# Kernel optimization log

Hardware: AMD Instinct MI355X
Metric: run time of the kernel (lower is better)

The kernel has to match this reference:

```python
import jax, jax.numpy as jnp
import numpy as np


def graph_conv(x, W, b, src, dst, n_nodes):
    """DGL GraphConv, norm='both', activation=relu.
    Pre-scale by out-degree^-1/2 of src, project (in>out so project first),
    sum-aggregate over edges, post-scale by in-degree^-1/2 of dst."""
    ones = jnp.ones(src.shape[0], dtype=x.dtype)
    deg_out = jax.ops.segment_sum(ones, src, num_segments=n_nodes)
    deg_in = jax.ops.segment_sum(ones, dst, num_segments=n_nodes)
    norm_src = jnp.clip(deg_out, 1.0, None) ** -0.5  # [N]
    norm_dst = jnp.clip(deg_in, 1.0, None) ** -0.5   # [N]
    h = x * norm_src[:, None]
    h = h @ W  # project first since in_feats > out_feats
    # message passing: gather src features, scatter-add into dst
    agg = jax.ops.segment_sum(h[src], dst, num_segments=n_nodes)  # [N, out]
    agg = agg * norm_dst[:, None]
    return jax.nn.relu(agg + b)


def setup_inputs() -> dict:
    key = jax.random.key(0)
    ks = jax.random.split(key, 6)
    N, E, D_IN, D_HID = 50000, 800000, 1024, 256
    x = jax.random.normal(ks[0], (N, D_IN), dtype=jnp.float32)
    src = jax.random.randint(ks[1], (E,), 0, N)
    dst = jax.random.randint(ks[2], (E,), 0, N)
    # Glorot-style init for weights
    W1 = jax.random.normal(ks[3], (D_IN, D_HID), dtype=jnp.float32) * (1.0 / np.sqrt(D_IN))
    b1 = jnp.zeros((D_HID,), dtype=jnp.float32)
    W2 = jax.random.normal(ks[4], (D_HID, 1), dtype=jnp.float32) * (1.0 / np.sqrt(D_HID))
    b2 = jnp.zeros((1,), dtype=jnp.float32)
    return {"x": x, "src": src, "dst": dst, "W1": W1, "b1": b1, "W2": W2, "b2": b2, "n_nodes": N}


def reference(x, src, dst, W1, b1, W2, b2, n_nodes):
    h = graph_conv(x, W1, b1, src, dst, n_nodes)   # [N, 256]
    out = graph_conv(h, W2, b2, src, dst, n_nodes)  # [N, 1]
    return out
```

## Files before the change

kernel.cpp:

```cpp
#include <hip/hip_runtime.h>
#include <hip/hip_bf16.h>

typedef __attribute__((ext_vector_type(8))) short bf16x8;
typedef __attribute__((ext_vector_type(4))) float f32x4;

static __device__ __forceinline__ short f2bf(float f) {
    unsigned u = __float_as_uint(f);
    unsigned r = (u + 0x7FFFu + ((u >> 16) & 1u)) >> 16;
    return (short)(unsigned short)r;
}
static __device__ __forceinline__ float bf2f(short s) {
    return __uint_as_float(((unsigned)(unsigned short)s) << 16);
}

static __device__ __forceinline__ void gload16(const void* g, void* l) {
    __builtin_amdgcn_global_load_lds((const __attribute__((address_space(1))) unsigned int*)g,
                                     (__attribute__((address_space(3))) unsigned int*)l, 16, 0, 0);
}

static __device__ __forceinline__ bf16x8 cvt8(const float4 lo, const float4 hi) {
    __hip_bfloat162 p0 = __float22bfloat162_rn(make_float2(lo.x, lo.y));
    __hip_bfloat162 p1 = __float22bfloat162_rn(make_float2(lo.z, lo.w));
    __hip_bfloat162 p2 = __float22bfloat162_rn(make_float2(hi.x, hi.y));
    __hip_bfloat162 p3 = __float22bfloat162_rn(make_float2(hi.z, hi.w));
    short2 s0 = *(short2*)&p0, s1 = *(short2*)&p1, s2 = *(short2*)&p2, s3 = *(short2*)&p3;
    bf16x8 r = {s0.x, s0.y, s1.x, s1.y, s2.x, s2.y, s3.x, s3.y};
    return r;
}

__global__ void deg_kernel(const int* __restrict__ src, const int* __restrict__ dst,
                           int* __restrict__ deg_out, int* __restrict__ deg_in, int E) {
    int e = blockIdx.x * blockDim.x + threadIdx.x;
    if (e < E) {
        atomicAdd(&deg_out[src[e]], 1);
        atomicAdd(&deg_in[dst[e]], 1);
    }
}

__global__ void norm_kernel(const int* __restrict__ deg_out, const int* __restrict__ deg_in,
                            float* __restrict__ ns, float* __restrict__ nd, int N) {
    int i = blockIdx.x * blockDim.x + threadIdx.x;
    if (i < N) {
        ns[i] = rsqrtf((float)max(deg_out[i], 1));
        nd[i] = rsqrtf((float)max(deg_in[i], 1));
    }
}

__global__ void scan_part1(const int* __restrict__ deg, int* __restrict__ bsum, int N) {
    __shared__ int red[256];
    int i = blockIdx.x * 256 + threadIdx.x;
    red[threadIdx.x] = (i < N) ? deg[i] : 0;
    __syncthreads();
    for (int off = 128; off > 0; off >>= 1) {
        if (threadIdx.x < off) red[threadIdx.x] += red[threadIdx.x + off];
        __syncthreads();
    }
    if (threadIdx.x == 0) bsum[blockIdx.x] = red[0];
}

__global__ void scan_part2(const int* __restrict__ bsum, int* __restrict__ bsum_ex, int NB,
                           int* __restrict__ offsets, int N, int E) {
    __shared__ int s[256];
    int t = threadIdx.x;
    int v = (t < NB) ? bsum[t] : 0;
    s[t] = v;
    __syncthreads();
    for (int off = 1; off < 256; off <<= 1) {
        int u = (t >= off) ? s[t - off] : 0;
        __syncthreads();
        s[t] += u;
        __syncthreads();
    }
    bsum_ex[t] = s[t] - v;
    if (t == 0) offsets[N] = E;
}

__global__ void scan_part3(const int* __restrict__ deg, const int* __restrict__ bsum_ex,
                           int* __restrict__ offsets, int N) {
    __shared__ int s[256];
    int t = threadIdx.x, i = blockIdx.x * 256 + t;
    int v = (i < N) ? deg[i] : 0;
    s[t] = v;
    __syncthreads();
    for (int off = 1; off < 256; off <<= 1) {
        int u = (t >= off) ? s[t - off] : 0;
        __syncthreads();
        s[t] += u;
        __syncthreads();
    }
    if (i < N) offsets[i] = bsum_ex[blockIdx.x] + s[t] - v;
}

__global__ void scatter_kernel(const int* __restrict__ src, const int* __restrict__ dst,
                               const int* __restrict__ offsets, int* __restrict__ cursor,
                               int* __restrict__ bucket, int E) {
    int e = blockIdx.x * blockDim.x + threadIdx.x;
    if (e < E) {
        int d = dst[e];
        int p = atomicAdd(&cursor[d], 1);
        bucket[offsets[d] + p] = src[e];
    }
}

__global__ __launch_bounds__(1024) void transpose_w1(const float* __restrict__ W1,
                                                     short* __restrict__ Wt) {
    __shared__ short tile[32][33];
    int k0 = blockIdx.x * 32, n0 = blockIdx.y * 32;
    int tx = threadIdx.x & 31, ty = threadIdx.x >> 5;
    tile[ty][tx] = f2bf(W1[(size_t)(k0 + ty) * 256 + (n0 + tx)]);
    __syncthreads();
    Wt[(size_t)(n0 + ty) * 1024 + (k0 + tx)] = tile[tx][ty];
}

#define BM 64
#define BN 128
#define BK 32
#define CSTR 136

union SMem {
    struct {
        short A[BM * BK];
        short B[BN * BK];
    } s;
    short C[BM * CSTR];
};

__global__ __launch_bounds__(256, 6) void gemm1_kernel(const float* __restrict__ x,
                                                       const short* __restrict__ Wt,
                                                       const float* __restrict__ norm_src,
                                                       short* __restrict__ hb, int M) {
    __shared__ __align__(16) SMem sm;
    __shared__ float ns_lds[BM];
    const int tid  = threadIdx.x;
    const int lane = tid & 63;
    const int wave = tid >> 6;
    const int quad = lane >> 4;
    const int mrow = lane & 15;
    const int wm = (wave >> 1) * 32;
    const int wn = (wave & 1) * 64;
    const int bm = blockIdx.x * BM;
    const int bn = blockIdx.y * BN;

    if (tid < BM) ns_lds[tid] = norm_src[min(bm + tid, M - 1)];

    f32x4 acc[2][4] = {};

    const int a_row = tid >> 2;
    const int a_chk = tid & 3;
    const float* a_src = x + (size_t)min(bm + a_row, M - 1) * 1024 + a_chk * 8;
    const bool a_ok = (bm + a_row < M);

    float4 a_lo, a_hi;
    a_lo = a_ok ? *(const float4*)(a_src + 0) : make_float4(0.f, 0.f, 0.f, 0.f);
    a_hi = a_ok ? *(const float4*)(a_src + 4) : make_float4(0.f, 0.f, 0.f, 0.f);

    for (int k0 = 0; k0 < 1024; k0 += BK) {
#pragma unroll
        for (int i = 0; i < 2; i++) {
            int nbase = wave * 32 + i * 16;
            int n = nbase + (lane >> 2);
            gload16(Wt + (size_t)(bn + n) * 1024 + k0 + (lane & 3) * 8, &sm.s.B[nbase * 32]);
        }
        *(bf16x8*)&sm.s.A[a_row * 32 + a_chk * 8] = cvt8(a_lo, a_hi);
        __syncthreads();

        if (k0 + BK < 1024) {
            a_lo = a_ok ? *(const float4*)(a_src + k0 + BK + 0) : make_float4(0.f, 0.f, 0.f, 0.f);
            a_hi = a_ok ? *(const float4*)(a_src + k0 + BK + 4) : make_float4(0.f, 0.f, 0.f, 0.f);
        }

        bf16x8 af[2], bfr[4];
#pragma unroll
        for (int mi = 0; mi < 2; mi++)
            af[mi] = *(const bf16x8*)&sm.s.A[(wm + mi * 16 + mrow) * 32 + quad * 8];
#pragma unroll
        for (int ni = 0; ni < 4; ni++)
            bfr[ni] = *(const bf16x8*)&sm.s.B[(wn + ni * 16 + mrow) * 32 + quad * 8];
#pragma unroll
        for (int mi = 0; mi < 2; mi++)
#pragma unroll
            for (int ni = 0; ni < 4; ni++)
                acc[mi][ni] = __builtin_amdgcn_mfma_f32_16x16x32_bf16(af[mi], bfr[ni], acc[mi][ni], 0, 0, 0);
        __syncthreads();
    }

#pragma unroll
    for (int mi = 0; mi < 2; mi++) {
#pragma unroll
        for (int reg = 0; reg < 4; reg++) {
            int row = wm + mi * 16 + quad * 4 + reg;
            float nsv = ns_lds[row];
#pragma unroll
            for (int ni = 0; ni < 4; ni++) {
                int col = wn + ni * 16 + mrow;
                sm.C[row * CSTR + col] = f2bf(acc[mi][ni][reg] * nsv);
            }
        }
    }
    __syncthreads();
#pragma unroll
    for (int j = 0; j < 4; j++) {
        int row = (tid >> 4) + j * 16;
        int chunk = tid & 15;
        if (bm + row < M) {
            int4 v = *(const int4*)&sm.C[row * CSTR + chunk * 8];
            *(int4*)(hb + (size_t)(bm + row) * 256 + bn + chunk * 8) = v;
        }
    }
}

__global__ __launch_bounds__(256) void agg1_kernel(const short* __restrict__ hb,
                                                   const int* __restrict__ bucket,
                                                   const int* __restrict__ offsets,
                                                   const float* __restrict__ norm_dst,
                                                   const float* __restrict__ norm_src,
                                                   const float* __restrict__ b1,
                                                   const float* __restrict__ W2,
                                                   float* __restrict__ z, int N) {
    int wave = threadIdx.x >> 6;
    int lane = threadIdx.x & 63;
    int node = blockIdx.x * 4 + wave;
    if (node >= N) return;
    int beg = offsets[node], end = offsets[node + 1];
    float a0 = 0.f, a1 = 0.f, a2 = 0.f, a3 = 0.f;
    int e = beg;
    for (; e + 7 < end; e += 8) {
        short4 v[8];
#pragma unroll
        for (int j = 0; j < 8; j++)
            v[j] = *(const short4*)(hb + (size_t)bucket[e + j] * 256 + lane * 4);
#pragma unroll
        for (int j = 0; j < 8; j++) {
            a0 += bf2f(v[j].x); a1 += bf2f(v[j].y);
            a2 += bf2f(v[j].z); a3 += bf2f(v[j].w);
        }
    }
    for (; e < end; e++) {
        short4 v0 = *(const short4*)(hb + (size_t)bucket[e] * 256 + lane * 4);
        a0 += bf2f(v0.x); a1 += bf2f(v0.y); a2 += bf2f(v0.z); a3 += bf2f(v0.w);
    }
    float nd = norm_dst[node];
    float4 bb = *(const float4*)(b1 + lane * 4);
    float o0 = fmaxf(a0 * nd + bb.x, 0.f);
    float o1 = fmaxf(a1 * nd + bb.y, 0.f);
    float o2 = fmaxf(a2 * nd + bb.z, 0.f);
    float o3 = fmaxf(a3 * nd + bb.w, 0.f);
    float4 w = *(const float4*)(W2 + lane * 4);
    float p = o0 * w.x + o1 * w.y + o2 * w.z + o3 * w.w;
#pragma unroll
    for (int off = 32; off > 0; off >>= 1) p += __shfl_xor(p, off, 64);
    if (lane == 0) z[node] = p * norm_src[node];
}

__global__ void agg2_kernel(const float* __restrict__ z, const int* __restrict__ bucket,
                            const int* __restrict__ offsets, const float* __restrict__ norm_dst,
                            const float* __restrict__ b2, float* __restrict__ out, int N) {
    int i = blockIdx.x * blockDim.x + threadIdx.x;
    if (i >= N) return;
    int beg = offsets[i], end = offsets[i + 1];
    float s = 0.f;
    for (int e = beg; e < end; e++) s += z[bucket[e]];
    out[i] = fmaxf(s * norm_dst[i] + b2[0], 0.f);
}

extern "C" void kernel_launch(void* const* d_in, const int* in_sizes, int n_in,
                              void* d_out, int out_size, void* d_ws, size_t ws_size,
                              hipStream_t stream) {
    const int D_HID = in_sizes[4];
    const int D_IN  = in_sizes[3] / D_HID;
    const int N     = in_sizes[0] / D_IN;
    const int E     = in_sizes[1];

    const float* x   = (const float*)d_in[0];
    const int*   src = (const int*)d_in[1];
    const int*   dst = (const int*)d_in[2];
    const float* W1  = (const float*)d_in[3];
    const float* b1  = (const float*)d_in[4];
    const float* W2  = (const float*)d_in[5];
    const float* b2  = (const float*)d_in[6];
    float* out = (float*)d_out;

    char* p = (char*)d_ws;
    auto alloc = [&](size_t bytes) {
        void* r = (void*)p;
        p += (bytes + 255) & ~(size_t)255;
        return r;
    };
    int*   deg_out  = (int*)alloc((size_t)N * 4);
    int*   deg_in   = (int*)alloc((size_t)N * 4);
    int*   cursor   = (int*)alloc((size_t)N * 4);
    float* norm_src = (float*)alloc((size_t)N * 4);
    float* norm_dst = (float*)alloc((size_t)N * 4);
    int*   offsets  = (int*)alloc((size_t)(N + 1) * 4);
    int*   bucket   = (int*)alloc((size_t)E * 4);
    short* Wt       = (short*)alloc((size_t)D_IN * D_HID * 2);
    short* hb       = (short*)alloc((size_t)N * D_HID * 2);
    float* z        = (float*)alloc((size_t)N * 4);
    int*   bsum     = (int*)alloc(256 * 4);
    int*   bsum_ex  = (int*)alloc(256 * 4);

    const int NB = (N + 255) / 256;

    hipMemsetAsync(deg_out, 0, (size_t)N * 4, stream);
    hipMemsetAsync(deg_in,  0, (size_t)N * 4, stream);
    hipMemsetAsync(cursor,  0, (size_t)N * 4, stream);

    deg_kernel<<<(E + 255) / 256, 256, 0, stream>>>(src, dst, deg_out, deg_in, E);
    norm_kernel<<<(N + 255) / 256, 256, 0, stream>>>(deg_out, deg_in, norm_src, norm_dst, N);
    scan_part1<<<NB, 256, 0, stream>>>(deg_in, bsum, N);
    scan_part2<<<1, 256, 0, stream>>>(bsum, bsum_ex, NB, offsets, N, E);
    scan_part3<<<NB, 256, 0, stream>>>(deg_in, bsum_ex, offsets, N);
    scatter_kernel<<<(E + 255) / 256, 256, 0, stream>>>(src, dst, offsets, cursor, bucket, E);
    transpose_w1<<<dim3(D_IN / 32, D_HID / 32), 1024, 0, stream>>>(W1, Wt);
    gemm1_kernel<<<dim3((N + BM - 1) / BM, D_HID / BN), 256, 0, stream>>>(x, Wt, norm_src, hb, N);
    agg1_kernel<<<(N + 3) / 4, 256, 0, stream>>>(hb, bucket, offsets, norm_dst, norm_src, b1, W2, z, N);
    agg2_kernel<<<(N + 255) / 256, 256, 0, stream>>>(z, bucket, offsets, norm_dst, b2, out, N);
}
```

Before: 526.2 us.

## Load full-width x tile once per block and stream W1 from registers

New measurement: 558.8 us. 1.06x slower.

```diff
diff --git a/kernel.cpp b/kernel.cpp
--- a/kernel.cpp
+++ b/kernel.cpp
@@ -12,12 +12,10 @@
 static __device__ __forceinline__ float bf2f(short s) {
     return __uint_as_float(((unsigned)(unsigned short)s) << 16);
 }
-
-static __device__ __forceinline__ void gload16(const void* g, void* l) {
-    __builtin_amdgcn_global_load_lds((const __attribute__((address_space(1))) unsigned int*)g,
-                                     (__attribute__((address_space(3))) unsigned int*)l, 16, 0, 0);
-}
-
+static __device__ __forceinline__ float4 nt_load4(const float* p) {
+    f32x4 v = __builtin_nontemporal_load((const f32x4*)p);
+    return make_float4(v[0], v[1], v[2], v[3]);
+}
 static __device__ __forceinline__ bf16x8 cvt8(const float4 lo, const float4 hi) {
     __hip_bfloat162 p0 = __float22bfloat162_rn(make_float2(lo.x, lo.y));
     __hip_bfloat162 p1 = __float22bfloat162_rn(make_float2(lo.z, lo.w));
@@ -112,20 +110,15 @@
     Wt[(size_t)(n0 + ty) * 1024 + (k0 + tx)] = tile[tx][ty];
 }
 
-#define BM 64
-#define BN 128
-#define BK 32
-#define CSTR 136
+#define BM 32
+#define CSTR 264
 
 union SMem {
-    struct {
-        short A[BM * BK];
-        short B[BN * BK];
-    } s;
+    short A[BM * 1024];
     short C[BM * CSTR];
 };
 
-__global__ __launch_bounds__(256, 6) void gemm1_kernel(const float* __restrict__ x,
+__global__ __launch_bounds__(256, 2) void gemm1_kernel(const float* __restrict__ x,
                                                        const short* __restrict__ Wt,
                                                        const float* __restrict__ norm_src,
                                                        short* __restrict__ hb, int M) {
@@ -136,59 +129,75 @@
     const int wave = tid >> 6;
     const int quad = lane >> 4;
     const int mrow = lane & 15;
-    const int wm = (wave >> 1) * 32;
-    const int wn = (wave & 1) * 64;
-    const int bm = blockIdx.x * BM;
-    const int bn = blockIdx.y * BN;
+    const int bm   = blockIdx.x * BM;
 
     if (tid < BM) ns_lds[tid] = norm_src[min(bm + tid, M - 1)];
 
+#pragma unroll
+    for (int half = 0; half < 2; half++) {
+        float4 lo[8], hi[8];
+#pragma unroll
+        for (int t = 0; t < 8; t++) {
+            int idx = half * 8 + t;
+            int r   = wave * 8 + (idx >> 1);
+            int s   = idx & 1;
+            const float* p = x + (size_t)min(bm + r, M - 1) * 1024 + s * 512 + lane * 8;
+            lo[t] = nt_load4(p);
+            hi[t] = nt_load4(p + 4);
+        }
+#pragma unroll
+        for (int t = 0; t < 8; t++) {
+            int idx = half * 8 + t;
+            int r   = wave * 8 + (idx >> 1);
+            int s   = idx & 1;
+            int c   = s * 64 + lane;
+            int cs  = c ^ (r & 7);
+            *(bf16x8*)((char*)sm.A + r * 2048 + cs * 16) = cvt8(lo[t], hi[t]);
+        }
+    }
+    __syncthreads();
+
     f32x4 acc[2][4] = {};
-
-    const int a_row = tid >> 2;
-    const int a_chk = tid & 3;
-    const float* a_src = x + (size_t)min(bm + a_row, M - 1) * 1024 + a_chk * 8;
-    const bool a_ok = (bm + a_row < M);
-
-    float4 a_lo, a_hi;
-    a_lo = a_ok ? *(const float4*)(a_src + 0) : make_float4(0.f, 0.f, 0.f, 0.f);
-    a_hi = a_ok ? *(const float4*)(a_src + 4) : make_float4(0.f, 0.f, 0.f, 0.f);
-
-    for (int k0 = 0; k0 < 1024; k0 += BK) {
-#pragma unroll
-        for (int i = 0; i < 2; i++) {
-            int nbase = wave * 32 + i * 16;
-            int n = nbase + (lane >> 2);
-            gload16(Wt + (size_t)(bn + n) * 1024 + k0 + (lane & 3) * 8, &sm.s.B[nbase * 32]);
-        }
-        *(bf16x8*)&sm.s.A[a_row * 32 + a_chk * 8] = cvt8(a_lo, a_hi);
-        __syncthreads();
-
-        if (k0 + BK < 1024) {
-            a_lo = a_ok ? *(const float4*)(a_src + k0 + BK + 0) : make_float4(0.f, 0.f, 0.f, 0.f);
-            a_hi = a_ok ? *(const float4*)(a_src + k0 + BK + 4) : make_float4(0.f, 0.f, 0.f, 0.f);
-        }
-
-        bf16x8 af[2], bfr[4];
+    const int wn = wave * 64;
+    const short* wB = Wt + (size_t)(wn + mrow) * 1024 + quad * 8;
+
+    bf16x8 bA[2][2], bB[2][4];
+#pragma unroll
+    for (int ni = 0; ni < 4; ni++)
+        bB[0][ni] = *(const bf16x8*)(wB + (size_t)ni * 16 * 1024);
+#pragma unroll
+    for (int mi = 0; mi < 2; mi++) {
+        int r = mi * 16 + mrow;
+        bA[0][mi] = *(const bf16x8*)((char*)sm.A + r * 2048 + ((quad ^ (r & 7)) * 16));
+    }
+
+    for (int k0 = 0; k0 < 1024; k0 += 32) {
+        int cur = (k0 >> 5) & 1, nxt = cur ^ 1;
+        if (k0 + 32 < 1024) {
+            int k1 = k0 + 32;
+#pragma unroll
+            for (int ni = 0; ni < 4; ni++)
+                bB[nxt][ni] = *(const bf16x8*)(wB + (size_t)ni * 16 * 1024 + k1);
+#pragma unroll
+            for (int mi = 0; mi < 2; mi++) {
+                int r = mi * 16 + mrow;
+                int c = (k1 >> 3) + quad;
+                bA[nxt][mi] = *(const bf16x8*)((char*)sm.A + r * 2048 + ((c ^ (r & 7)) * 16));
+            }
+        }
 #pragma unroll
         for (int mi = 0; mi < 2; mi++)
-            af[mi] = *(const bf16x8*)&sm.s.A[(wm + mi * 16 + mrow) * 32 + quad * 8];
-#pragma unroll
-        for (int ni = 0; ni < 4; ni++)
-            bfr[ni] = *(const bf16x8*)&sm.s.B[(wn + ni * 16 + mrow) * 32 + quad * 8];
-#pragma unroll
-        for (int mi = 0; mi < 2; mi++)
 #pragma unroll
             for (int ni = 0; ni < 4; ni++)
-                acc[mi][ni] = __builtin_amdgcn_mfma_f32_16x16x32_bf16(af[mi], bfr[ni], acc[mi][ni], 0, 0, 0);
-        __syncthreads();
-    }
-
+                acc[mi][ni] = __builtin_amdgcn_mfma_f32_16x16x32_bf16(bA[cur][mi], bB[cur][ni], acc[mi][ni], 0, 0, 0);
+    }
+
+    __syncthreads();
 #pragma unroll
     for (int mi = 0; mi < 2; mi++) {
 #pragma unroll
         for (int reg = 0; reg < 4; reg++) {
-            int row = wm + mi * 16 + quad * 4 + reg;
+            int row = mi * 16 + quad * 4 + reg;
             float nsv = ns_lds[row];
 #pragma unroll
             for (int ni = 0; ni < 4; ni++) {
@@ -198,13 +207,15 @@
         }
     }
     __syncthreads();
-#pragma unroll
-    for (int j = 0; j < 4; j++) {
-        int row = (tid >> 4) + j * 16;
-        int chunk = tid & 15;
+    {
+        int row = tid >> 3;
         if (bm + row < M) {
-            int4 v = *(const int4*)&sm.C[row * CSTR + chunk * 8];
-            *(int4*)(hb + (size_t)(bm + row) * 256 + bn + chunk * 8) = v;
+#pragma unroll
+            for (int j = 0; j < 4; j++) {
+                int chunk = (tid & 7) + j * 8;
+                int4 v = *(const int4*)&sm.C[row * CSTR + chunk * 8];
+                *(int4*)(hb + (size_t)(bm + row) * 256 + chunk * 8) = v;
+            }
         }
     }
 }
@@ -301,9 +312,9 @@
 
     const int NB = (N + 255) / 256;
 
-    hipMemsetAsync(deg_out, 0, (size_t)N * 4, stream);
-    hipMemsetAsync(deg_in,  0, (size_t)N * 4, stream);
-    hipMemsetAsync(cursor,  0, (size_t)N * 4, stream);
+    (void)hipMemsetAsync(deg_out, 0, (size_t)N * 4, stream);
+    (void)hipMemsetAsync(deg_in,  0, (size_t)N * 4, stream);
+    (void)hipMemsetAsync(cursor,  0, (size_t)N * 4, stream);
 
     deg_kernel<<<(E + 255) / 256, 256, 0, stream>>>(src, dst, deg_out, deg_in, E);
     norm_kernel<<<(N + 255) / 256, 256, 0, stream>>>(deg_out, deg_in, norm_src, norm_dst, N);
@@ -312,7 +323,7 @@
     scan_part3<<<NB, 256, 0, stream>>>(deg_in, bsum_ex, offsets, N);
     scatter_kernel<<<(E + 255) / 256, 256, 0, stream>>>(src, dst, offsets, cursor, bucket, E);
     transpose_w1<<<dim3(D_IN / 32, D_HID / 32), 1024, 0, stream>>>(W1, Wt);
-    gemm1_kernel<<<dim3((N + BM - 1) / BM, D_HID / BN), 256, 0, stream>>>(x, Wt, norm_src, hb, N);
+    gemm1_kernel<<<(N + BM - 1) / BM, 256, 0, stream>>>(x, Wt, norm_src, hb, N);
     agg1_kernel<<<(N + 3) / 4, 256, 0, stream>>>(hb, bucket, offsets, norm_dst, norm_src, b1, W2, z, N);
     agg2_kernel<<<(N + 255) / 256, 256, 0, stream>>>(z, bucket, offsets, norm_dst, b2, out, N);
 }
```
